# Kernel tuning notes

Measured on AMD Instinct MI355X. Metric: run time of the kernel, lower is better.

The kernel has to match this reference:

```python
import jax, jax.numpy as jnp
import numpy as np

B, C, H, W, K = 32, 64, 112, 112, 5


def setup_inputs() -> dict:
    key = jax.random.key(0)
    kx, = jax.random.split(key, 1)
    x = jax.random.uniform(kx, (B, C, H, W), dtype=jnp.float32)
    # parameters per BioNorm.reset_parameters()
    sigma = jnp.ones((C,), jnp.float32)
    pow_p = jnp.full((C,), 2.0, jnp.float32)
    sum_kernel = jnp.full((C, 1, K, K), 1.0 / (K * K), jnp.float32)
    weight = jnp.ones((C,), jnp.float32)
    bias = jnp.zeros((C,), jnp.float32)
    return {"x": x, "sigma": sigma, "pow_p": pow_p, "sum_kernel": sum_kernel,
            "weight": weight, "bias": bias}


def _bionorm(x, sigma, pow_p, sum_kernel, weight, bias):
    s = sigma.reshape(1, -1, 1, 1)
    p = pow_p.reshape(1, -1, 1, 1)
    w = weight.reshape(1, -1, 1, 1)
    b = bias.reshape(1, -1, 1, 1)
    xp = x ** p  # [B,C,H,W]
    # depthwise (grouped) conv, VALID padding -> [B,C,H-K+1,W-K+1]
    sf = jax.lax.conv_general_dilated(
        xp, sum_kernel, window_strides=(1, 1), padding='VALID',
        feature_group_count=C,
        dimension_numbers=('NCHW', 'OIHW', 'NCHW'))
    hks = K // 2
    # replicate-pad back to [B,C,H,W]
    sf = jnp.pad(sf, ((0, 0), (0, 0), (hks, hks), (hks, hks)), mode='edge')
    den = s ** p + sf
    return w * xp / den + b


def reference(x, sigma, pow_p, sum_kernel, weight, bias):
    return _bionorm(x, sigma, pow_p, sum_kernel, weight, bias)
```

## Files before the change

kernel.cpp:

```cpp
#include <hip/hip_runtime.h>


#define Cch 64
#define Hh 112
#define Ww 112
#define CPB 36
#define RPS 9

__global__ __launch_bounds__(256) void bionorm_kernel(
    const float* __restrict__ x, const float* __restrict__ sigma,
    const float* __restrict__ pow_p, const float* __restrict__ sum_kernel,
    const float* __restrict__ weight, const float* __restrict__ bias,
    float* __restrict__ out)
{
    const int bx  = blockIdx.x;
    const int b   = blockIdx.z;
    const int tid = threadIdx.x;
    const int c   = blockIdx.y * 2 + (tid >> 7);
    const int t   = tid & 127;

    const int ss = t >> 5;
    const int g  = t & 31;
    if (g >= 27) return;

    const float p  = pow_p[c];
    const float sg = sigma[c];
    const float wc = weight[c];
    const float bc = bias[c];
    const bool  p2 = (p == 2.0f);
    const float sp = p2 ? sg * sg : __powf(sg, p);

    float kw[25];
    const float* kp = sum_kernel + c * 25;
    #pragma unroll
    for (int j = 0; j < 25; ++j) kw[j] = kp[j];
    bool uni = true;
    #pragma unroll
    for (int j = 1; j < 25; ++j) uni = uni && (kw[j] == kw[0]);

    const float* xplane = x + ((size_t)(b * Cch + c)) * (Hh * Ww);
    float* oplane = out + ((size_t)(b * Cch + c)) * (Hh * Ww);

    const int cs   = 2 + bx * CPB + ss * RPS;
    const int col0 = 4 * g;

    float win[5][8];

    #define CVT8(SL, VA, VB) { \
        if (p2) { \
            win[SL][0] = VA.x * VA.x; win[SL][1] = VA.y * VA.y; \
            win[SL][2] = VA.z * VA.z; win[SL][3] = VA.w * VA.w; \
            win[SL][4] = VB.x * VB.x; win[SL][5] = VB.y * VB.y; \
            win[SL][6] = VB.z * VB.z; win[SL][7] = VB.w * VB.w; \
        } else { \
            win[SL][0] = __powf(VA.x, p); win[SL][1] = __powf(VA.y, p); \
            win[SL][2] = __powf(VA.z, p); win[SL][3] = __powf(VA.w, p); \
            win[SL][4] = __powf(VB.x, p); win[SL][5] = __powf(VB.y, p); \
            win[SL][6] = __powf(VB.z, p); win[SL][7] = __powf(VB.w, p); \
        } }

    #define EMITROW(GR, SL) { \
        float* orw_ = oplane + (GR) * Ww; \
        *(float2*)(orw_ + col0 + 2) = make_float2(fmaf(wc * win[SL][2], d0, bc), \
                                                  fmaf(wc * win[SL][3], d1, bc)); \
        *(float2*)(orw_ + col0 + 4) = make_float2(fmaf(wc * win[SL][4], d2, bc), \
                                                  fmaf(wc * win[SL][5], d3, bc)); \
        if (g == 0)  *(float2*)(orw_)       = make_float2(fmaf(wc * win[SL][0], d0, bc), \
                                                          fmaf(wc * win[SL][1], d0, bc)); \
        if (g == 26) *(float2*)(orw_ + 110) = make_float2(fmaf(wc * win[SL][6], d3, bc), \
                                                          fmaf(wc * win[SL][7], d3, bc)); }

    #define EDGEEMITS() { \
        const int cgl = cs + k; \
        EMITROW(cgl, (k + 2) % 5) \
        if (k == 0 && cs == 2) {            \
            EMITROW(0, 0) \
            EMITROW(1, 1) \
        } \
        if (k == RPS - 1 && cgl == 109) {   \
            EMITROW(110, (k + 3) % 5) \
            EMITROW(111, (k + 4) % 5) \
        } }

    {
        const float4 a0 = *(const float4*)(xplane + (cs - 2) * Ww + col0);
        const float4 b0 = *(const float4*)(xplane + (cs - 2) * Ww + col0 + 4);
        const float4 a1 = *(const float4*)(xplane + (cs - 1) * Ww + col0);
        const float4 b1 = *(const float4*)(xplane + (cs - 1) * Ww + col0 + 4);
        const float4 a2 = *(const float4*)(xplane + (cs    ) * Ww + col0);
        const float4 b2 = *(const float4*)(xplane + (cs    ) * Ww + col0 + 4);
        const float4 a3 = *(const float4*)(xplane + (cs + 1) * Ww + col0);
        const float4 b3 = *(const float4*)(xplane + (cs + 1) * Ww + col0 + 4);
        CVT8(0, a0, b0) CVT8(1, a1, b1) CVT8(2, a2, b2) CVT8(3, a3, b3)
    }
    float4 A0 = *(const float4*)(xplane + (cs + 2) * Ww + col0);
    float4 A1 = *(const float4*)(xplane + (cs + 2) * Ww + col0 + 4);

    if (uni) {
        const float k0 = kw[0];
        float v[8];
        #pragma unroll
        for (int tt = 0; tt < 8; ++tt)
            v[tt] = win[0][tt] + win[1][tt] + win[2][tt] + win[3][tt];

        #pragma unroll
        for (int k = 0; k < RPS; ++k) {
            const int nr  = cs + k + 3;
            const int nrc = nr > 111 ? 111 : nr;
            const float4 B0 = *(const float4*)(xplane + nrc * Ww + col0);
            const float4 B1 = *(const float4*)(xplane + nrc * Ww + col0 + 4);

            const int sl = (k + 4) % 5;
            CVT8(sl, A0, A1)
            #pragma unroll
            for (int tt = 0; tt < 8; ++tt) v[tt] += win[sl][tt];

            const float h0 = ((v[0] + v[1]) + (v[2] + v[3])) + v[4];
            const float h1 = h0 - v[0] + v[5];
            const float h2 = h1 - v[1] + v[6];
            const float h3 = h2 - v[2] + v[7];

            const float d0 = __builtin_amdgcn_rcpf(fmaf(k0, h0, sp));
            const float d1 = __builtin_amdgcn_rcpf(fmaf(k0, h1, sp));
            const float d2 = __builtin_amdgcn_rcpf(fmaf(k0, h2, sp));
            const float d3 = __builtin_amdgcn_rcpf(fmaf(k0, h3, sp));

            EDGEEMITS()

            if (k < RPS - 1) {
                #pragma unroll
                for (int tt = 0; tt < 8; ++tt) v[tt] -= win[k % 5][tt];
            }
            A0 = B0; A1 = B1;
        }
    } else {
        #pragma unroll
        for (int k = 0; k < RPS; ++k) {
            const int nr  = cs + k + 3;
            const int nrc = nr > 111 ? 111 : nr;
            const float4 B0 = *(const float4*)(xplane + nrc * Ww + col0);
            const float4 B1 = *(const float4*)(xplane + nrc * Ww + col0 + 4);

            CVT8((k + 4) % 5, A0, A1)

            float S0 = 0.f, S1 = 0.f, S2 = 0.f, S3 = 0.f;
            #pragma unroll
            for (int dy = 0; dy < 5; ++dy) {
                const int sl = (k + dy) % 5;
                #pragma unroll
                for (int dx = 0; dx < 5; ++dx) {
                    const float kv = kw[dy * 5 + dx];
                    S0 = fmaf(kv, win[sl][dx + 0], S0);
                    S1 = fmaf(kv, win[sl][dx + 1], S1);
                    S2 = fmaf(kv, win[sl][dx + 2], S2);
                    S3 = fmaf(kv, win[sl][dx + 3], S3);
                }
            }

            const float d0 = __builtin_amdgcn_rcpf(sp + S0);
            const float d1 = __builtin_amdgcn_rcpf(sp + S1);
            const float d2 = __builtin_amdgcn_rcpf(sp + S2);
            const float d3 = __builtin_amdgcn_rcpf(sp + S3);

            EDGEEMITS()

            A0 = B0; A1 = B1;
        }
    }
    #undef CVT8
    #undef EMITROW
    #undef EDGEEMITS
}

extern "C" void kernel_launch(void* const* d_in, const int* in_sizes, int n_in,
                              void* d_out, int out_size, void* d_ws, size_t ws_size,
                              hipStream_t stream) {
    const float* x          = (const float*)d_in[0];
    const float* sigma      = (const float*)d_in[1];
    const float* pow_p      = (const float*)d_in[2];
    const float* sum_kernel = (const float*)d_in[3];
    const float* weight     = (const float*)d_in[4];
    const float* bias       = (const float*)d_in[5];
    float* out = (float*)d_out;

    dim3 grid(3, Cch / 2, 32);
    dim3 block(256);
    bionorm_kernel<<<grid, block, 0, stream>>>(x, sigma, pow_p, sum_kernel,
                                               weight, bias, out);
}
```

Before: 199.6 us.

## Split rows into finer tiles with upfront loads and nontemporal stores

Each 32-lane group now handles 3 output rows instead of 9, and the grid grows from 3 to 9 row tiles per plane. All 7 input rows a thread needs are loaded and converted up front instead of being streamed through a rolling 5-row window. Output stores become nontemporal. This gives more blocks and more memory parallelism, at the cost of reading more halo rows again (7 loads per 3 output rows instead of 13 per 9) and holding more registers per thread.

```diff
diff --git a/kernel.cpp b/kernel.cpp
--- a/kernel.cpp
+++ b/kernel.cpp
@@ -4,8 +4,10 @@
 #define Cch 64
 #define Hh 112
 #define Ww 112
-#define CPB 36
-#define RPS 9
+#define RT 9
+#define RPS 3
+
+typedef float v2f __attribute__((ext_vector_type(2)));
 
 __global__ __launch_bounds__(256) void bionorm_kernel(
     const float* __restrict__ x, const float* __restrict__ sigma,
@@ -18,9 +20,8 @@
     const int tid = threadIdx.x;
     const int c   = blockIdx.y * 2 + (tid >> 7);
     const int t   = tid & 127;
-
-    const int ss = t >> 5;
-    const int g  = t & 31;
+    const int ss  = t >> 5;
+    const int g   = t & 31;
     if (g >= 27) return;
 
     const float p  = pow_p[c];
@@ -41,119 +42,93 @@
     const float* xplane = x + ((size_t)(b * Cch + c)) * (Hh * Ww);
     float* oplane = out + ((size_t)(b * Cch + c)) * (Hh * Ww);
 
-    const int cs   = 2 + bx * CPB + ss * RPS;
+    const int cb   = 2 + bx * (4 * RPS) + ss * RPS;
+    const int rr0  = cb - 2;
     const int col0 = 4 * g;
 
-    float win[5][8];
+    float4 ra[7], rb[7];
+    #pragma unroll
+    for (int i = 0; i < 7; ++i) {
+        const float* rp = xplane + (rr0 + i) * Ww + col0;
+        ra[i] = *(const float4*)(rp);
+        rb[i] = *(const float4*)(rp + 4);
+    }
 
-    #define CVT8(SL, VA, VB) { \
-        if (p2) { \
-            win[SL][0] = VA.x * VA.x; win[SL][1] = VA.y * VA.y; \
-            win[SL][2] = VA.z * VA.z; win[SL][3] = VA.w * VA.w; \
-            win[SL][4] = VB.x * VB.x; win[SL][5] = VB.y * VB.y; \
-            win[SL][6] = VB.z * VB.z; win[SL][7] = VB.w * VB.w; \
-        } else { \
-            win[SL][0] = __powf(VA.x, p); win[SL][1] = __powf(VA.y, p); \
-            win[SL][2] = __powf(VA.z, p); win[SL][3] = __powf(VA.w, p); \
-            win[SL][4] = __powf(VB.x, p); win[SL][5] = __powf(VB.y, p); \
-            win[SL][6] = __powf(VB.z, p); win[SL][7] = __powf(VB.w, p); \
-        } }
+    float win[7][8];
+    #pragma unroll
+    for (int i = 0; i < 7; ++i) {
+        if (p2) {
+            win[i][0] = ra[i].x * ra[i].x; win[i][1] = ra[i].y * ra[i].y;
+            win[i][2] = ra[i].z * ra[i].z; win[i][3] = ra[i].w * ra[i].w;
+            win[i][4] = rb[i].x * rb[i].x; win[i][5] = rb[i].y * rb[i].y;
+            win[i][6] = rb[i].z * rb[i].z; win[i][7] = rb[i].w * rb[i].w;
+        } else {
+            win[i][0] = __powf(ra[i].x, p); win[i][1] = __powf(ra[i].y, p);
+            win[i][2] = __powf(ra[i].z, p); win[i][3] = __powf(ra[i].w, p);
+            win[i][4] = __powf(rb[i].x, p); win[i][5] = __powf(rb[i].y, p);
+            win[i][6] = __powf(rb[i].z, p); win[i][7] = __powf(rb[i].w, p);
+        }
+    }
 
     #define EMITROW(GR, SL) { \
         float* orw_ = oplane + (GR) * Ww; \
-        *(float2*)(orw_ + col0 + 2) = make_float2(fmaf(wc * win[SL][2], d0, bc), \
-                                                  fmaf(wc * win[SL][3], d1, bc)); \
-        *(float2*)(orw_ + col0 + 4) = make_float2(fmaf(wc * win[SL][4], d2, bc), \
-                                                  fmaf(wc * win[SL][5], d3, bc)); \
-        if (g == 0)  *(float2*)(orw_)       = make_float2(fmaf(wc * win[SL][0], d0, bc), \
-                                                          fmaf(wc * win[SL][1], d0, bc)); \
-        if (g == 26) *(float2*)(orw_ + 110) = make_float2(fmaf(wc * win[SL][6], d3, bc), \
-                                                          fmaf(wc * win[SL][7], d3, bc)); }
+        v2f e0_ = {fmaf(wc * win[SL][2], d0, bc), fmaf(wc * win[SL][3], d1, bc)}; \
+        v2f e1_ = {fmaf(wc * win[SL][4], d2, bc), fmaf(wc * win[SL][5], d3, bc)}; \
+        __builtin_nontemporal_store(e0_, (v2f*)(orw_ + col0 + 2)); \
+        __builtin_nontemporal_store(e1_, (v2f*)(orw_ + col0 + 4)); \
+        if (g == 0) { \
+            v2f eL_ = {fmaf(wc * win[SL][0], d0, bc), fmaf(wc * win[SL][1], d0, bc)}; \
+            __builtin_nontemporal_store(eL_, (v2f*)(orw_)); } \
+        if (g == 26) { \
+            v2f eR_ = {fmaf(wc * win[SL][6], d3, bc), fmaf(wc * win[SL][7], d3, bc)}; \
+            __builtin_nontemporal_store(eR_, (v2f*)(orw_ + 110)); } }
 
     #define EDGEEMITS() { \
-        const int cgl = cs + k; \
-        EMITROW(cgl, (k + 2) % 5) \
-        if (k == 0 && cs == 2) {            \
-            EMITROW(0, 0) \
-            EMITROW(1, 1) \
-        } \
-        if (k == RPS - 1 && cgl == 109) {   \
-            EMITROW(110, (k + 3) % 5) \
-            EMITROW(111, (k + 4) % 5) \
-        } }
-
-    {
-        const float4 a0 = *(const float4*)(xplane + (cs - 2) * Ww + col0);
-        const float4 b0 = *(const float4*)(xplane + (cs - 2) * Ww + col0 + 4);
-        const float4 a1 = *(const float4*)(xplane + (cs - 1) * Ww + col0);
-        const float4 b1 = *(const float4*)(xplane + (cs - 1) * Ww + col0 + 4);
-        const float4 a2 = *(const float4*)(xplane + (cs    ) * Ww + col0);
-        const float4 b2 = *(const float4*)(xplane + (cs    ) * Ww + col0 + 4);
-        const float4 a3 = *(const float4*)(xplane + (cs + 1) * Ww + col0);
-        const float4 b3 = *(const float4*)(xplane + (cs + 1) * Ww + col0 + 4);
-        CVT8(0, a0, b0) CVT8(1, a1, b1) CVT8(2, a2, b2) CVT8(3, a3, b3)
-    }
-    float4 A0 = *(const float4*)(xplane + (cs + 2) * Ww + col0);
-    float4 A1 = *(const float4*)(xplane + (cs + 2) * Ww + col0 + 4);
+        if (k == 0 && cb == 2)       { EMITROW(0, 0)   EMITROW(1, 1) } \
+        if (k == 2 && cb == 107)     { EMITROW(110, 5) EMITROW(111, 6) } }
 
     if (uni) {
         const float k0 = kw[0];
-        float v[8];
+        float vs[8];
         #pragma unroll
         for (int tt = 0; tt < 8; ++tt)
-            v[tt] = win[0][tt] + win[1][tt] + win[2][tt] + win[3][tt];
+            vs[tt] = ((win[0][tt] + win[1][tt]) + (win[2][tt] + win[3][tt]))
+                     + win[4][tt];
 
         #pragma unroll
         for (int k = 0; k < RPS; ++k) {
-            const int nr  = cs + k + 3;
-            const int nrc = nr > 111 ? 111 : nr;
-            const float4 B0 = *(const float4*)(xplane + nrc * Ww + col0);
-            const float4 B1 = *(const float4*)(xplane + nrc * Ww + col0 + 4);
-
-            const int sl = (k + 4) % 5;
-            CVT8(sl, A0, A1)
-            #pragma unroll
-            for (int tt = 0; tt < 8; ++tt) v[tt] += win[sl][tt];
-
-            const float h0 = ((v[0] + v[1]) + (v[2] + v[3])) + v[4];
-            const float h1 = h0 - v[0] + v[5];
-            const float h2 = h1 - v[1] + v[6];
-            const float h3 = h2 - v[2] + v[7];
+            const float h0 = ((vs[0] + vs[1]) + (vs[2] + vs[3])) + vs[4];
+            const float h1 = h0 - vs[0] + vs[5];
+            const float h2 = h1 - vs[1] + vs[6];
+            const float h3 = h2 - vs[2] + vs[7];
 
             const float d0 = __builtin_amdgcn_rcpf(fmaf(k0, h0, sp));
             const float d1 = __builtin_amdgcn_rcpf(fmaf(k0, h1, sp));
             const float d2 = __builtin_amdgcn_rcpf(fmaf(k0, h2, sp));
             const float d3 = __builtin_amdgcn_rcpf(fmaf(k0, h3, sp));
 
+            EMITROW(cb + k, k + 2)
             EDGEEMITS()
 
             if (k < RPS - 1) {
                 #pragma unroll
-                for (int tt = 0; tt < 8; ++tt) v[tt] -= win[k % 5][tt];
+                for (int tt = 0; tt < 8; ++tt)
+                    vs[tt] += win[k + 5][tt] - win[k][tt];
             }
-            A0 = B0; A1 = B1;
         }
     } else {
         #pragma unroll
         for (int k = 0; k < RPS; ++k) {
-            const int nr  = cs + k + 3;
-            const int nrc = nr > 111 ? 111 : nr;
-            const float4 B0 = *(const float4*)(xplane + nrc * Ww + col0);
-            const float4 B1 = *(const float4*)(xplane + nrc * Ww + col0 + 4);
-
-            CVT8((k + 4) % 5, A0, A1)
-
             float S0 = 0.f, S1 = 0.f, S2 = 0.f, S3 = 0.f;
             #pragma unroll
             for (int dy = 0; dy < 5; ++dy) {
-                const int sl = (k + dy) % 5;
                 #pragma unroll
                 for (int dx = 0; dx < 5; ++dx) {
                     const float kv = kw[dy * 5 + dx];
-                    S0 = fmaf(kv, win[sl][dx + 0], S0);
-                    S1 = fmaf(kv, win[sl][dx + 1], S1);
-                    S2 = fmaf(kv, win[sl][dx + 2], S2);
-                    S3 = fmaf(kv, win[sl][dx + 3], S3);
+                    S0 = fmaf(kv, win[k + dy][dx + 0], S0);
+                    S1 = fmaf(kv, win[k + dy][dx + 1], S1);
+                    S2 = fmaf(kv, win[k + dy][dx + 2], S2);
+                    S3 = fmaf(kv, win[k + dy][dx + 3], S3);
                 }
             }
 
@@ -162,12 +137,10 @@
             const float d2 = __builtin_amdgcn_rcpf(sp + S2);
             const float d3 = __builtin_amdgcn_rcpf(sp + S3);
 
+            EMITROW(cb + k, k + 2)
             EDGEEMITS()
-
-            A0 = B0; A1 = B1;
         }
     }
-    #undef CVT8
     #undef EMITROW
     #undef EDGEEMITS
 }
@@ -183,7 +156,7 @@
     const float* bias       = (const float*)d_in[5];
     float* out = (float*)d_out;
 
-    dim3 grid(3, Cch / 2, 32);
+    dim3 grid(RT, Cch / 2, 32);
     dim3 block(256);
     bionorm_kernel<<<grid, block, 0, stream>>>(x, sigma, pow_p, sum_kernel,
                                                weight, bias, out);
```

Result: no change. 195.7 us (-2.0%).
